# Optimization experiments

Hardware: AMD Instinct MI355X
Metric: run time of the kernel (lower is better)

## Reference

```python
import jax, jax.numpy as jnp
import numpy as np

B, S, D, K = 1024, 256, 128, 26


def setup_inputs() -> dict:
    key = jax.random.key(0)
    k1, k2, k3 = jax.random.split(key, 3)
    input_x = jax.random.normal(k1, (B, S, D), dtype=jnp.float32)
    weights = jax.random.normal(k2, (K, D), dtype=jnp.float32) * 0.1
    transition = jax.random.normal(k3, (K, K), dtype=jnp.float32) * 0.1
    return {"input_x": input_x, "weights": weights, "transition": transition}


def reference(input_x, weights, transition):
    """Batched Viterbi (max-sum) decoding, identical math to max_sum_solution.max_sum.

    Score of a path y: sum_t <x_t, W[y_t]> + sum_t T[y_t, y_{t+1}].
    Returns the argmax label sequence per batch element, shape [B, S], int32.
    """
    # emissions: [B, S, K]
    emis = jnp.einsum('bsd,kd->bsk', input_x, weights)

    def step(delta, e_t):
        # delta: [B, K] best score ending at each label at time t-1
        # scores over (prev=j, next=k): delta[b,j] + T[j,k]
        scores = delta[:, :, None] + transition[None, :, :]  # [B, K, K]
        bp = jnp.argmax(scores, axis=1).astype(jnp.int32)     # [B, K] best prev
        new_delta = jnp.max(scores, axis=1) + e_t             # [B, K]
        return new_delta, bp

    delta0 = emis[:, 0, :]
    # scan over time steps 1..S-1
    deltaT, backptrs = jax.lax.scan(step, delta0, jnp.swapaxes(emis[:, 1:, :], 0, 1))
    # backptrs: [S-1, B, K]

    last = jnp.argmax(deltaT, axis=-1).astype(jnp.int32)  # [B]

    def backtrack(nxt, bp_t):
        # nxt: [B] label at time t+1; bp_t: [B, K]
        prev = jnp.take_along_axis(bp_t, nxt[:, None], axis=1)[:, 0]
        return prev, prev

    _, path_prefix = jax.lax.scan(backtrack, last, backptrs, reverse=True)
    # path_prefix: [S-1, B] labels for times 0..S-2
    path = jnp.concatenate([path_prefix, last[None, :]], axis=0)  # [S, B]
    return jnp.swapaxes(path, 0, 1)  # [B, S]
```

## Files before the change

kernel.cpp:

```cpp
#include <hip/hip_runtime.h>

#define B_ 1024
#define S_ 256
#define D_ 128
#define K_ 26
#define EST 27

__global__ __launch_bounds__(128, 2) void crf_pc(
    const float* __restrict__ X, const float* __restrict__ W,
    const float* __restrict__ Tr, int* __restrict__ out)
{
  __shared__ __align__(16) float e_lds[S_ * EST];
  __shared__ __align__(16) float ring[2][D_];
  __shared__ __align__(16) float pub[28];
  __shared__ unsigned char bp[K_][260];
  __shared__ int prog[4];

  const int tid  = threadIdx.x;
  const int lane = tid & 63;
  const int b    = blockIdx.x;

  if (tid == 0) prog[0] = 0;
  __syncthreads();

  if (tid >= 64) {
    const int j  = lane & 31;
    const int h  = lane >> 5;
    const int jc = (j < K_) ? j : (K_ - 1);
    float w[64];
    {
      const float4* wp = reinterpret_cast<const float4*>(W + jc * D_ + h * 64);
#pragma unroll
      for (int q = 0; q < 16; ++q) {
        float4 v4 = wp[q];
        w[4*q+0] = v4.x; w[4*q+1] = v4.y; w[4*q+2] = v4.z; w[4*q+3] = v4.w;
      }
    }
    const float* xb = X + (size_t)b * (S_ * D_);
    float2 g = *reinterpret_cast<const float2*>(xb + 2 * lane);
    *reinterpret_cast<float2*>(&ring[0][2 * lane]) = g;
    g = *reinterpret_cast<const float2*>(xb + D_ + 2 * lane);
    asm volatile("" ::: "memory");

    for (int r = 0; r < S_; ++r) {
      const int cur = r & 1;
      float a0 = 0.f, a1 = 0.f, a2 = 0.f, a3 = 0.f;
      const float4* rp = reinterpret_cast<const float4*>(&ring[cur][h * 64]);
#pragma unroll
      for (int q = 0; q < 16; ++q) {
        float4 x4 = rp[q];
        a0 = fmaf(x4.x, w[4*q+0], a0);
        a1 = fmaf(x4.y, w[4*q+1], a1);
        a2 = fmaf(x4.z, w[4*q+2], a2);
        a3 = fmaf(x4.w, w[4*q+3], a3);
      }
      float p = (a0 + a1) + (a2 + a3);
      float e = p + __shfl_xor(p, 32, 64);
      if (r + 1 < S_) *reinterpret_cast<float2*>(&ring[cur ^ 1][2 * lane]) = g;
      if (r + 2 < S_)
        g = *reinterpret_cast<const float2*>(xb + (size_t)(r + 2) * D_ + 2 * lane);
      if (h == 0 && j < K_) e_lds[r * EST + j] = e;
      asm volatile("" ::: "memory");
      if (lane == 0) *(volatile int*)&prog[0] = r + 1;
    }
    return;
  }

  const int jc = (lane < K_) ? lane : (K_ - 1);
  float tc[K_];
#pragma unroll
  for (int i = 0; i < K_; ++i) tc[i] = Tr[i * K_ + jc];

  volatile int* vprog = prog;
#define WAIT_ROWS(n) do { while (*vprog < (n)) {} asm volatile("" ::: "memory"); } while (0)

  WAIT_ROWS(2);
  float delta = e_lds[jc];
  if (lane < 28) pub[lane] = -3.4e38f;
  if (lane < K_) pub[lane] = delta;
  asm volatile("" ::: "memory");

  float4 raw[7];
  {
    const float4* p = reinterpret_cast<const float4*>(pub);
#pragma unroll
    for (int q = 0; q < 7; ++q) raw[q] = p[q];
  }
  float ev_cur = e_lds[EST + jc];

  for (int ch = 0; ch < 16; ++ch) {
    const int tend = 16 * (ch + 1);
    const int need = (tend + 1 < S_) ? (tend + 1) : S_;
    WAIT_ROWS(need);
    for (int t = (ch == 0 ? 1 : 16 * ch); t < tend; ++t) {
      float v[K_ + 2];
#pragma unroll
      for (int q = 0; q < 7; ++q) {
        v[4*q+0] = raw[q].x; v[4*q+1] = raw[q].y;
        v[4*q+2] = raw[q].z; v[4*q+3] = raw[q].w;
      }
#pragma unroll
      for (int i = 0; i < K_; ++i) v[i] += tc[i];

      float m[9];
#pragma unroll
      for (int i = 0; i < 8; ++i)
        m[i] = fmaxf(fmaxf(v[3*i], v[3*i+1]), v[3*i+2]);
      m[8] = fmaxf(v[24], v[25]);
      float n0 = fmaxf(fmaxf(m[0], m[1]), m[2]);
      float n1 = fmaxf(fmaxf(m[3], m[4]), m[5]);
      float n2 = fmaxf(fmaxf(m[6], m[7]), m[8]);
      float best = fmaxf(fmaxf(n0, n1), n2);

      delta = best + ev_cur;

      if (lane < K_) pub[lane] = delta;
      asm volatile("" ::: "memory");
      {
        const float4* p = reinterpret_cast<const float4*>(pub);
#pragma unroll
        for (int q = 0; q < 7; ++q) raw[q] = p[q];
      }

      int tn = (t + 1 < S_) ? (t + 1) : (S_ - 1);
      ev_cur = e_lds[tn * EST + jc];

      int idx = 63;
#pragma unroll
      for (int i = K_ - 1; i >= 0; --i) idx = (v[i] == best) ? i : idx;
      if (lane < K_) bp[lane][t] = (unsigned char)idx;
    }
  }

  int last;
  {
    float v[K_];
#pragma unroll
    for (int q = 0; q < 7; ++q) {
      if (4*q+0 < K_) v[4*q+0] = raw[q].x;
      if (4*q+1 < K_) v[4*q+1] = raw[q].y;
      if (4*q+2 < K_) v[4*q+2] = raw[q].z;
      if (4*q+3 < K_) v[4*q+3] = raw[q].w;
    }
    float bf = v[0];
#pragma unroll
    for (int i = 1; i < K_; ++i) bf = fmaxf(bf, v[i]);
    int iA = 63;
#pragma unroll
    for (int i = K_ - 1; i >= 0; --i) iA = (v[i] == bf) ? i : iA;
    last = iA;
  }

  asm volatile("s_waitcnt lgkmcnt(0)" ::: "memory");

  unsigned char (*spec)[132] = reinterpret_cast<unsigned char (*)[132]>(e_lds);
  int* path_s = reinterpret_cast<int*>(reinterpret_cast<char*>(e_lds) + 4096);

  {
    int c = (lane < K_) ? lane : last;
    for (int k = 0; k < 128; ++k) {
      int t = (lane < K_) ? (128 - k) : (255 - k);
      bool act = (lane < K_) || (lane == 63 && k <= 126);
      if (act) {
        c = bp[c][t];
        if (lane < K_) spec[lane][t - 1] = (unsigned char)c;
        else if (t >= 129) path_s[t - 1] = c;
      }
    }
  }
  asm volatile("s_waitcnt lgkmcnt(0)" ::: "memory");

  {
    int sstar = path_s[128];
#pragma unroll
    for (int q2 = 0; q2 < 2; ++q2) {
      int t = q2 * 64 + lane;
      path_s[t] = (int)spec[sstar][t];
    }
    if (lane == 0) path_s[S_ - 1] = last;
  }
  asm volatile("s_waitcnt lgkmcnt(0)" ::: "memory");

  int* o = out + (size_t)b * S_;
#pragma unroll
  for (int q2 = 0; q2 < 4; ++q2) o[q2 * 64 + lane] = path_s[q2 * 64 + lane];
#undef WAIT_ROWS
}

extern "C" void kernel_launch(void* const* d_in, const int* in_sizes, int n_in,
                              void* d_out, int out_size, void* d_ws, size_t ws_size,
                              hipStream_t stream) {
  (void)in_sizes; (void)n_in; (void)out_size; (void)d_ws; (void)ws_size;
  const float* X  = (const float*)d_in[0];
  const float* W  = (const float*)d_in[1];
  const float* Tr = (const float*)d_in[2];
  int* outp = (int*)d_out;
  crf_pc<<<B_, 128, 0, stream>>>(X, W, Tr, outp);
}
```

Measured before the change: 120.9 us.

## Offload Viterbi backpointer argmax to a third wavefront via delta history ring

Adds a third wavefront that reads past delta vectors from a 32-slot LDS history ring and recomputes the argmax backpointers, so the serial critical-path wave only does the max recurrence. The recurrence is also rewritten with packed two-wide float max operations to shorten the dependency chain. Progress counters synchronize producer and consumer and guard the ring against overwrite. This costs more threads and LDS per block, changes occupancy to three blocks per CU, and adds spin-wait coordination.

```diff
diff --git a/kernel.cpp b/kernel.cpp
--- a/kernel.cpp
+++ b/kernel.cpp
@@ -4,26 +4,30 @@
 #define S_ 256
 #define D_ 128
 #define K_ 26
-#define EST 27
-
-__global__ __launch_bounds__(128, 2) void crf_pc(
+#define WIN 32
+
+typedef float v2f __attribute__((ext_vector_type(2)));
+#define EMAX(a, b) __builtin_elementwise_max((a), (b))
+
+__global__ __launch_bounds__(192, 3) void crf_pc3(
     const float* __restrict__ X, const float* __restrict__ W,
     const float* __restrict__ Tr, int* __restrict__ out)
 {
-  __shared__ __align__(16) float e_lds[S_ * EST];
+  __shared__ __align__(16) float e_lds[S_ * K_];
+  __shared__ __align__(16) float hist[WIN * 28];
+  __shared__ unsigned char bp[K_][260];
   __shared__ __align__(16) float ring[2][D_];
-  __shared__ __align__(16) float pub[28];
-  __shared__ unsigned char bp[K_][260];
-  __shared__ int prog[4];
+  __shared__ int prog[8];
 
   const int tid  = threadIdx.x;
   const int lane = tid & 63;
+  const int wv   = tid >> 6;
   const int b    = blockIdx.x;
 
-  if (tid == 0) prog[0] = 0;
+  if (tid == 0) { prog[0] = 0; prog[1] = -1; prog[2] = 0; }
   __syncthreads();
 
-  if (tid >= 64) {
+  if (wv == 1) {
     const int j  = lane & 31;
     const int h  = lane >> 5;
     const int jc = (j < K_) ? j : (K_ - 1);
@@ -59,98 +63,131 @@
       if (r + 1 < S_) *reinterpret_cast<float2*>(&ring[cur ^ 1][2 * lane]) = g;
       if (r + 2 < S_)
         g = *reinterpret_cast<const float2*>(xb + (size_t)(r + 2) * D_ + 2 * lane);
-      if (h == 0 && j < K_) e_lds[r * EST + j] = e;
+      if (h == 0 && j < K_) e_lds[r * K_ + j] = e;
       asm volatile("" ::: "memory");
       if (lane == 0) *(volatile int*)&prog[0] = r + 1;
     }
     return;
   }
 
+  if (wv == 2) {
+    const int jc = (lane < K_) ? lane : (K_ - 1);
+    v2f tc2[13];
+#pragma unroll
+    for (int q = 0; q < 13; ++q)
+      tc2[q] = (v2f){Tr[(2*q) * K_ + jc], Tr[(2*q+1) * K_ + jc]};
+
+    int seen = -1;
+    for (int tp = 1; tp < S_; ++tp) {
+      if (seen < tp - 1) {
+        do { seen = *(volatile int*)&prog[1]; } while (seen < tp - 1);
+        asm volatile("" ::: "memory");
+      }
+      const float4* hp =
+          reinterpret_cast<const float4*>(&hist[((tp - 1) & (WIN - 1)) * 28]);
+      float4 d4[7];
+#pragma unroll
+      for (int q = 0; q < 7; ++q) d4[q] = hp[q];
+      float vs[26];
+      {
+        const float* df = reinterpret_cast<const float*>(d4);
+        const float* tf = reinterpret_cast<const float*>(tc2);
+#pragma unroll
+        for (int i = 0; i < K_; ++i) vs[i] = df[i] + tf[i];
+      }
+      float m[9];
+#pragma unroll
+      for (int i = 0; i < 8; ++i) m[i] = fmaxf(fmaxf(vs[3*i], vs[3*i+1]), vs[3*i+2]);
+      m[8] = fmaxf(vs[24], vs[25]);
+      float best = fmaxf(fmaxf(fmaxf(m[0], m[1]), m[2]),
+                   fmaxf(fmaxf(m[3], m[4]), m[5]));
+      best = fmaxf(best, fmaxf(fmaxf(m[6], m[7]), m[8]));
+      int idx = 63;
+#pragma unroll
+      for (int i = K_ - 1; i >= 0; --i) idx = (vs[i] == best) ? i : idx;
+      if (lane < K_) bp[lane][tp] = (unsigned char)idx;
+      asm volatile("" ::: "memory");
+      if ((tp & 7) == 7 || tp == S_ - 1)
+        if (lane == 0) *(volatile int*)&prog[2] = tp;
+    }
+    return;
+  }
+
   const int jc = (lane < K_) ? lane : (K_ - 1);
-  float tc[K_];
-#pragma unroll
-  for (int i = 0; i < K_; ++i) tc[i] = Tr[i * K_ + jc];
-
-  volatile int* vprog = prog;
-#define WAIT_ROWS(n) do { while (*vprog < (n)) {} asm volatile("" ::: "memory"); } while (0)
-
-  WAIT_ROWS(2);
+  v2f tc2[13];
+#pragma unroll
+  for (int q = 0; q < 13; ++q)
+    tc2[q] = (v2f){Tr[(2*q) * K_ + jc], Tr[(2*q+1) * K_ + jc]};
+
+  volatile int* veprog = &prog[0];
+#define WAIT_E(n) do { while (*veprog < (n)) {} asm volatile("" ::: "memory"); } while (0)
+
+  WAIT_E(2);
   float delta = e_lds[jc];
-  if (lane < 28) pub[lane] = -3.4e38f;
-  if (lane < K_) pub[lane] = delta;
+  if (lane < K_) hist[lane] = delta;
   asm volatile("" ::: "memory");
+  if (lane == 0) *(volatile int*)&prog[1] = 0;
 
   float4 raw[7];
   {
-    const float4* p = reinterpret_cast<const float4*>(pub);
+    const float4* p = reinterpret_cast<const float4*>(&hist[0]);
 #pragma unroll
     for (int q = 0; q < 7; ++q) raw[q] = p[q];
   }
-  float ev_cur = e_lds[EST + jc];
+  float ev_cur = e_lds[K_ + jc];
 
   for (int ch = 0; ch < 16; ++ch) {
-    const int tend = 16 * (ch + 1);
-    const int need = (tend + 1 < S_) ? (tend + 1) : S_;
-    WAIT_ROWS(need);
-    for (int t = (ch == 0 ? 1 : 16 * ch); t < tend; ++t) {
-      float v[K_ + 2];
-#pragma unroll
-      for (int q = 0; q < 7; ++q) {
-        v[4*q+0] = raw[q].x; v[4*q+1] = raw[q].y;
-        v[4*q+2] = raw[q].z; v[4*q+3] = raw[q].w;
-      }
-#pragma unroll
-      for (int i = 0; i < K_; ++i) v[i] += tc[i];
-
-      float m[9];
-#pragma unroll
-      for (int i = 0; i < 8; ++i)
-        m[i] = fmaxf(fmaxf(v[3*i], v[3*i+1]), v[3*i+2]);
-      m[8] = fmaxf(v[24], v[25]);
-      float n0 = fmaxf(fmaxf(m[0], m[1]), m[2]);
-      float n1 = fmaxf(fmaxf(m[3], m[4]), m[5]);
-      float n2 = fmaxf(fmaxf(m[6], m[7]), m[8]);
-      float best = fmaxf(fmaxf(n0, n1), n2);
+    const int t0 = 16 * ch, tend = t0 + 16;
+    const int needE = (tend + 1 < S_) ? (tend + 1) : S_;
+    WAIT_E(needE);
+    if (t0 >= 32) {
+      while (*(volatile int*)&prog[2] < t0 - 16) {}
+      asm volatile("" ::: "memory");
+    }
+    for (int t = (ch == 0 ? 1 : t0); t < tend; ++t) {
+      const v2f* rp2 = reinterpret_cast<const v2f*>(raw);
+      v2f v0 = rp2[0] + tc2[0],  v1 = rp2[1] + tc2[1],  v2 = rp2[2] + tc2[2];
+      v2f v3 = rp2[3] + tc2[3],  v4 = rp2[4] + tc2[4],  v5 = rp2[5] + tc2[5];
+      v2f v6 = rp2[6] + tc2[6],  v7 = rp2[7] + tc2[7],  v8 = rp2[8] + tc2[8];
+      v2f v9 = rp2[9] + tc2[9],  va = rp2[10] + tc2[10], vb = rp2[11] + tc2[11];
+      v2f vc = rp2[12] + tc2[12];
+      v2f a0 = EMAX(v0, v1), a1 = EMAX(v2, v3), a2 = EMAX(v4, v5);
+      v2f a3 = EMAX(v6, v7), a4 = EMAX(v8, v9), a5 = EMAX(va, vb);
+      v2f b0 = EMAX(a0, a1), b1 = EMAX(a2, a3), b2 = EMAX(a4, a5);
+      v2f c0 = EMAX(b0, b1), c1 = EMAX(b2, vc);
+      v2f z  = EMAX(c0, c1);
+      float best = fmaxf(z.x, z.y);
 
       delta = best + ev_cur;
 
-      if (lane < K_) pub[lane] = delta;
+      const int slot = (t & (WIN - 1)) * 28;
+      if (lane < K_) hist[slot + lane] = delta;
       asm volatile("" ::: "memory");
       {
-        const float4* p = reinterpret_cast<const float4*>(pub);
+        const float4* p = reinterpret_cast<const float4*>(&hist[slot]);
 #pragma unroll
         for (int q = 0; q < 7; ++q) raw[q] = p[q];
       }
-
       int tn = (t + 1 < S_) ? (t + 1) : (S_ - 1);
-      ev_cur = e_lds[tn * EST + jc];
-
-      int idx = 63;
-#pragma unroll
-      for (int i = K_ - 1; i >= 0; --i) idx = (v[i] == best) ? i : idx;
-      if (lane < K_) bp[lane][t] = (unsigned char)idx;
+      ev_cur = e_lds[tn * K_ + jc];
+      if ((t & 3) == 3)
+        if (lane == 0) *(volatile int*)&prog[1] = t;
     }
   }
 
   int last;
   {
-    float v[K_];
-#pragma unroll
-    for (int q = 0; q < 7; ++q) {
-      if (4*q+0 < K_) v[4*q+0] = raw[q].x;
-      if (4*q+1 < K_) v[4*q+1] = raw[q].y;
-      if (4*q+2 < K_) v[4*q+2] = raw[q].z;
-      if (4*q+3 < K_) v[4*q+3] = raw[q].w;
-    }
-    float bf = v[0];
-#pragma unroll
-    for (int i = 1; i < K_; ++i) bf = fmaxf(bf, v[i]);
+    const float* vf = reinterpret_cast<const float*>(raw);
+    float bf = vf[0];
+#pragma unroll
+    for (int i = 1; i < K_; ++i) bf = fmaxf(bf, vf[i]);
     int iA = 63;
 #pragma unroll
-    for (int i = K_ - 1; i >= 0; --i) iA = (v[i] == bf) ? i : iA;
+    for (int i = K_ - 1; i >= 0; --i) iA = (vf[i] == bf) ? i : iA;
     last = iA;
   }
 
+  while (*(volatile int*)&prog[2] < S_ - 1) {}
   asm volatile("s_waitcnt lgkmcnt(0)" ::: "memory");
 
   unsigned char (*spec)[132] = reinterpret_cast<unsigned char (*)[132]>(e_lds);
@@ -184,7 +221,7 @@
   int* o = out + (size_t)b * S_;
 #pragma unroll
   for (int q2 = 0; q2 < 4; ++q2) o[q2 * 64 + lane] = path_s[q2 * 64 + lane];
-#undef WAIT_ROWS
+#undef WAIT_E
 }
 
 extern "C" void kernel_launch(void* const* d_in, const int* in_sizes, int n_in,
@@ -195,5 +232,5 @@
   const float* W  = (const float*)d_in[1];
   const float* Tr = (const float*)d_in[2];
   int* outp = (int*)d_out;
-  crf_pc<<<B_, 128, 0, stream>>>(X, W, Tr, outp);
+  crf_pc3<<<B_, 192, 0, stream>>>(X, W, Tr, outp);
 }
```

Measured after the change: 155.1 us. +28.2%, slower.

## Split Viterbi backtrack into parallel speculative segments across both waves

Applied to the files above, without the earlier changes.

The serial backtrack is split into four 64-step segments. The idle producer wave computes two speculative segments while the consumer wave computes one speculative segment plus the true tail chain. The segments are stitched together using the label at each boundary. This halves the length of the serial dependent LDS-load chain, at the cost of extra LDS flag handshakes between waves and more scratch space in LDS.

```diff
diff --git a/kernel.cpp b/kernel.cpp
--- a/kernel.cpp
+++ b/kernel.cpp
@@ -14,13 +14,21 @@
   __shared__ __align__(16) float ring[2][D_];
   __shared__ __align__(16) float pub[28];
   __shared__ unsigned char bp[K_][260];
-  __shared__ int prog[4];
+  __shared__ int prog[8];
 
   const int tid  = threadIdx.x;
   const int lane = tid & 63;
   const int b    = blockIdx.x;
 
-  if (tid == 0) prog[0] = 0;
+  unsigned char (*specC)[64] =
+      reinterpret_cast<unsigned char (*)[64]>(reinterpret_cast<char*>(e_lds));
+  unsigned char (*specB)[64] =
+      reinterpret_cast<unsigned char (*)[64]>(reinterpret_cast<char*>(e_lds) + 2048);
+  unsigned char (*specA)[64] =
+      reinterpret_cast<unsigned char (*)[64]>(reinterpret_cast<char*>(e_lds) + 4096);
+  int* path_s = reinterpret_cast<int*>(reinterpret_cast<char*>(e_lds) + 6144);
+
+  if (tid == 0) { prog[0] = 0; prog[1] = 0; prog[2] = 0; }
   __syncthreads();
 
   if (tid >= 64) {
@@ -63,6 +71,29 @@
       asm volatile("" ::: "memory");
       if (lane == 0) *(volatile int*)&prog[0] = r + 1;
     }
+
+    while (*(volatile int*)&prog[1] == 0) __builtin_amdgcn_s_sleep(8);
+    asm volatile("" ::: "memory");
+
+    {
+      const int sl   = lane & 31;
+      const bool inB = (lane < K_);
+      const bool inA = (lane >= 32 && sl < K_);
+      int c = sl;
+      for (int k = 0; k < 64; ++k) {
+        if (inB) {
+          int t = 128 - k;
+          c = bp[c][t];
+          specB[sl][t - 1 - 64] = (unsigned char)c;
+        } else if (inA) {
+          int t = 64 - k;
+          c = bp[c][t];
+          specA[sl][t - 1] = (unsigned char)c;
+        }
+      }
+    }
+    asm volatile("s_waitcnt lgkmcnt(0)" ::: "memory");
+    if (lane == 0) *(volatile int*)&prog[2] = 1;
     return;
   }
 
@@ -152,31 +183,36 @@
   }
 
   asm volatile("s_waitcnt lgkmcnt(0)" ::: "memory");
-
-  unsigned char (*spec)[132] = reinterpret_cast<unsigned char (*)[132]>(e_lds);
-  int* path_s = reinterpret_cast<int*>(reinterpret_cast<char*>(e_lds) + 4096);
-
-  {
-    int c = (lane < K_) ? lane : last;
-    for (int k = 0; k < 128; ++k) {
-      int t = (lane < K_) ? (128 - k) : (255 - k);
-      bool act = (lane < K_) || (lane == 63 && k <= 126);
-      if (act) {
+  if (lane == 0) *(volatile int*)&prog[1] = 1;
+
+  {
+    const bool isC = (lane < K_);
+    const bool isR = (lane == 63);
+    int c = isC ? lane : last;
+    for (int k = 0; k < 64; ++k) {
+      if (isC) {
+        int t = 192 - k;
         c = bp[c][t];
-        if (lane < K_) spec[lane][t - 1] = (unsigned char)c;
-        else if (t >= 129) path_s[t - 1] = c;
+        specC[lane][t - 1 - 128] = (unsigned char)c;
+      } else if (isR && k <= 62) {
+        int t = 255 - k;
+        c = bp[c][t];
+        path_s[t - 1] = c;
       }
     }
   }
   asm volatile("s_waitcnt lgkmcnt(0)" ::: "memory");
 
-  {
-    int sstar = path_s[128];
-#pragma unroll
-    for (int q2 = 0; q2 < 2; ++q2) {
-      int t = q2 * 64 + lane;
-      path_s[t] = (int)spec[sstar][t];
-    }
+  while (*(volatile int*)&prog[2] == 0) {}
+  asm volatile("" ::: "memory");
+
+  {
+    int sC = path_s[192];
+    int sB = (int)specC[sC][0];
+    int sA = (int)specB[sB][0];
+    path_s[128 + lane] = (int)specC[sC][lane];
+    path_s[64 + lane]  = (int)specB[sB][lane];
+    path_s[lane]       = (int)specA[sA][lane];
     if (lane == 0) path_s[S_ - 1] = last;
   }
   asm volatile("s_waitcnt lgkmcnt(0)" ::: "memory");
```

After: 118.4 us. -2.1%, faster.
